# Kernel optimization log

Hardware: AMD Instinct MI355X
Metric: run time of the kernel (lower is better)

The kernel has to match this reference:

```python
import jax, jax.numpy as jnp
import numpy as np
import math

SCALES = (1, 2, 4)
GROUPS = 8
EPS = 1e-5
TEMPERATURE = 1.0


def bilinear_resize(x, out_h, out_w):
    # torch F.interpolate mode='bilinear', align_corners=False
    B, C, h, w = x.shape
    def coords(out, in_):
        c = (jnp.arange(out, dtype=x.dtype) + 0.5) * (in_ / out) - 0.5
        c = jnp.clip(c, 0.0, in_ - 1.0)
        i0 = jnp.floor(c).astype(jnp.int32)
        i1 = jnp.minimum(i0 + 1, in_ - 1)
        t = c - i0.astype(x.dtype)
        return i0, i1, t
    y0, y1, ty = coords(out_h, h)
    x0, x1, tx = coords(out_w, w)
    r0 = x[:, :, y0, :]
    r1 = x[:, :, y1, :]
    v00 = r0[:, :, :, x0]; v01 = r0[:, :, :, x1]
    v10 = r1[:, :, :, x0]; v11 = r1[:, :, :, x1]
    top = v00 * (1.0 - tx) + v01 * tx
    bot = v10 * (1.0 - tx) + v11 * tx
    return top * (1.0 - ty)[:, None] + bot * ty[:, None]


def group_norm(x, gamma, beta):
    B, C, H, W = x.shape
    xg = x.reshape(B, GROUPS, C // GROUPS, H, W)
    mu = xg.mean(axis=(2, 3, 4), keepdims=True)
    var = xg.var(axis=(2, 3, 4), keepdims=True)
    xn = ((xg - mu) * jax.lax.rsqrt(var + EPS)).reshape(B, C, H, W)
    return xn * gamma[None, :, None, None] + beta[None, :, None, None]


def setup_inputs() -> dict:
    key = jax.random.key(0)
    B, C, H, W = 4, 128, 64, 64
    inter = max(C // 4, 8)  # 32
    S = len(SCALES)
    ks = jax.random.split(key, 8)
    def xavier(k, shape, fan_in, fan_out):
        a = math.sqrt(6.0 / (fan_in + fan_out))
        return jax.random.uniform(k, shape, jnp.float32, -a, a)
    inp = {
        'x': jax.random.normal(ks[0], (B, C, H, W), jnp.float32),
        'gn_w': jnp.ones((S, C), jnp.float32),
        'gn_b': jnp.zeros((S, C), jnp.float32),
        'qw': xavier(ks[1], (S, inter, C), C, inter),
        'qb': jnp.zeros((S, inter), jnp.float32),
        'kw': xavier(ks[2], (S, inter, C), C, inter),
        'kb': jnp.zeros((S, inter), jnp.float32),
        'vw': xavier(ks[3], (S, inter, C), C, inter),
        'vb': jnp.zeros((S, inter), jnp.float32),
        'ow': xavier(ks[4], (S, C, inter), inter, C),
        'ob': jnp.zeros((S, C), jnp.float32),
        'gamma': jnp.full((S,), 0.1 / S, jnp.float32),
        'scale_weights': jnp.full((S,), 1.0 / S, jnp.float32),
    }
    return inp


def _forward(x, gn_w, gn_b, qw, qb, kw, kb, vw, vb, ow, ob, gamma, scale_weights):
    B, C, H, W = x.shape
    inter = qw.shape[1]
    inv_scale = 1.0 / (TEMPERATURE * math.sqrt(inter))
    outs = []
    for i, s in enumerate(SCALES):
        if s == 1:
            xs = x
        else:
            xs = x.reshape(B, C, H // s, s, W // s, s).mean(axis=(3, 5))
        h, w = xs.shape[2], xs.shape[3]
        N = h * w
        xn = group_norm(xs, gn_w[i], gn_b[i])
        # 1x1 convs as channel contractions
        q = (jnp.einsum('oc,bchw->bohw', qw[i], xn) + qb[i][None, :, None, None]).reshape(B, inter, N)
        k = (jnp.einsum('oc,bchw->bohw', kw[i], xn) + kb[i][None, :, None, None]).reshape(B, inter, N)
        v = (jnp.einsum('oc,bchw->bohw', vw[i], xn) + vb[i][None, :, None, None]).reshape(B, inter, N)
        logits = jnp.einsum('bin,bim->bnm', q, k) * inv_scale  # [B, N, N]
        attn = jax.nn.softmax(logits, axis=-1)
        att = jnp.einsum('bnm,bim->bin', attn, v).reshape(B, inter, h, w)
        o = jnp.einsum('ci,bihw->bchw', ow[i], att) + ob[i][None, :, None, None]
        y = gamma[i] * o + xs
        if s > 1:
            y = bilinear_resize(y, H, W)
        outs.append(y)
    wts = jax.nn.softmax(scale_weights, axis=0)
    fused = wts[0] * outs[0]
    for i in range(1, len(outs)):
        fused = fused + wts[i] * outs[i]
    return fused


def reference(x, gn_w, gn_b, qw, qb, kw, kb, vw, vb, ow, ob, gamma, scale_weights):
    return _forward(x, gn_w, gn_b, qw, qb, kw, kb, vw, vb, ow, ob, gamma, scale_weights)
```

## Files before the change

### kernel.cpp

```cpp
#include <hip/hip_runtime.h>
#include <math.h>

#define B 4
#define C 128
#define CPG 16
#define INTER 32
#define SPLIT 16
#define KS 4

#define N1 4096
#define N2 1024
#define N4 256

#define QOFF2 (B * N1 * 32)
#define QOFF4 (QOFF2 + B * N2 * 32)
#define QTOT  (QOFF4 + B * N4 * 32)
#define PAOFF2 (B * KS * 32 * N1)
#define PAOFF4 (PAOFF2 + B * KS * 32 * N2)
#define PATOT  (PAOFF4 + B * KS * 32 * N4)
#define PMOFF2 (B * KS * 2 * N1)
#define PMOFF4 (PMOFF2 + B * KS * 2 * N2)
#define PMTOT  (PMOFF4 + B * KS * 2 * N4)

typedef unsigned short ushort_t;
typedef __attribute__((ext_vector_type(8))) short short8;
typedef __attribute__((ext_vector_type(4))) short short4v;
typedef __attribute__((ext_vector_type(4))) float f32x4;

__device__ __forceinline__ ushort_t f2bf(float f) {
    union { float f; unsigned u; } x; x.f = f;
    unsigned r = x.u + 0x7fffu + ((x.u >> 16) & 1u);
    return (ushort_t)(r >> 16);
}

__device__ __forceinline__ void scale_wts(const float* __restrict__ sw,
                                          float& w0, float& w1, float& w2) {
    float a = sw[0], b = sw[1], c = sw[2];
    float m = fmaxf(a, fmaxf(b, c));
    float e0 = __expf(a - m), e1 = __expf(b - m), e2 = __expf(c - m);
    float inv = 1.0f / (e0 + e1 + e2);
    w0 = e0 * inv; w1 = e1 * inv; w2 = e2 * inv;
}

__device__ __forceinline__ void block_reduce_write(float s, float q,
                                                   float* __restrict__ dst2) {
    __shared__ float rs[256], rq[256];
    rs[threadIdx.x] = s; rq[threadIdx.x] = q;
    __syncthreads();
    for (int st = 128; st > 0; st >>= 1) {
        if (threadIdx.x < st) {
            rs[threadIdx.x] += rs[threadIdx.x + st];
            rq[threadIdx.x] += rq[threadIdx.x + st];
        }
        __syncthreads();
    }
    if (threadIdx.x == 0) { dst2[0] = rs[0]; dst2[1] = rq[0]; }
}

__global__ __launch_bounds__(256) void pool_stats_kernel(const float* __restrict__ x,
                                                         float* __restrict__ xs2,
                                                         float* __restrict__ xs4,
                                                         float* __restrict__ part) {
    int bid = blockIdx.x;
    if (bid < 512) {
        int sp = bid & 15, bg = bid >> 4;
        const float* base = x + ((bg * CPG) << 12) + sp * 4096;
        float s = 0.0f, q = 0.0f;
        for (int i = threadIdx.x; i < 4096; i += 256) {
            float v = base[i];
            s += v; q += v * v;
        }
        block_reduce_write(s, q, part + bid * 2);
    } else if (bid < 1024) {
        int blk = bid - 512;
        int sp = blk & 15, bg = blk >> 4;
        int bc = bg * CPG + sp;
        const float* src = x + (bc << 12);
        float* dst = xs2 + (bc << 10);
        float s = 0.0f, q = 0.0f;
        for (int p = threadIdx.x; p < 1024; p += 256) {
            int oy = p >> 5, ox = p & 31;
            const float* s2 = src + oy * 128 + ox * 2;
            float v = (s2[0] + s2[1] + s2[64] + s2[65]) * 0.25f;
            dst[p] = v; s += v; q += v * v;
        }
        block_reduce_write(s, q, part + 1024 + blk * 2);
    } else {
        int blk = bid - 1024;
        int sp = blk & 15, bg = blk >> 4;
        int bc = bg * CPG + sp;
        const float* src = x + (bc << 12);
        float* dst = xs4 + (bc << 8);
        int p = threadIdx.x & 255;
        int oy = p >> 4, ox = p & 15;
        const float* s4 = src + oy * 256 + ox * 4;
        float v = 0.0f;
        #pragma unroll
        for (int dy = 0; dy < 4; ++dy)
            #pragma unroll
            for (int dx = 0; dx < 4; ++dx) v += s4[dy * 64 + dx];
        v *= 0.0625f;
        dst[p] = v;
        block_reduce_write(v, v * v, part + 2048 + blk * 2);
    }
}

template <int N, int NSH>
__device__ __forceinline__ void qkv_body(int bi, const float* __restrict__ xs,
    const float* __restrict__ part,
    const float* __restrict__ gn_w, const float* __restrict__ gn_b,
    const float* __restrict__ qw, const float* __restrict__ qb,
    const float* __restrict__ kw, const float* __restrict__ kb,
    const float* __restrict__ vw, const float* __restrict__ vb,
    ushort_t* __restrict__ q_bf, ushort_t* __restrict__ k_bf, ushort_t* __restrict__ v_bf) {
    const int nc = N >> 8;
    int nchunk = bi % nc; bi /= nc;
    int og = bi & 3; bi >>= 2;
    int proj = bi % 3; int b = bi / 3;
    const float* wp = (proj == 0) ? qw : ((proj == 1) ? kw : vw);
    const float* bp = (proj == 0) ? qb : ((proj == 1) ? kb : vb);
    __shared__ float wl[8 * 128];
    __shared__ float2 ss[128];
    {
        int t = threadIdx.x;
        #pragma unroll
        for (int r = 0; r < 4; ++r) {
            int e = r * 256 + t;
            int o = e >> 7, c0 = e & 127;
            wl[c0 * 8 + o] = wp[(og * 8 + o) * C + c0];
        }
        if (t < 128) {
            int c = t;
            int bg = b * 8 + (c >> 4);
            float s = 0.0f, q = 0.0f;
            #pragma unroll
            for (int sp = 0; sp < SPLIT; ++sp) {
                s += part[(bg * SPLIT + sp) * 2];
                q += part[(bg * SPLIT + sp) * 2 + 1];
            }
            float inv = 1.0f / (float)(CPG << NSH);
            float mu = s * inv;
            float var = q * inv - mu * mu;
            float a = rsqrtf(var + 1e-5f) * gn_w[c];
            float2 r; r.x = a; r.y = gn_b[c] - mu * a;
            ss[c] = r;
        }
    }
    __syncthreads();
    int n = nchunk * 256 + threadIdx.x;
    const float* xb = xs + ((size_t)(b * C) << NSH) + n;
    float acc[8];
    #pragma unroll
    for (int o = 0; o < 8; ++o) acc[o] = bp[og * 8 + o];
    #pragma unroll 2
    for (int c0 = 0; c0 < C; ++c0) {
        float raw = xb[(size_t)c0 << NSH];
        float2 s2 = ss[c0];
        float xv = fmaf(s2.x, raw, s2.y);
        const float4* wr = (const float4*)&wl[c0 * 8];
        float4 w0 = wr[0], w1 = wr[1];
        acc[0] += w0.x * xv; acc[1] += w0.y * xv; acc[2] += w0.z * xv; acc[3] += w0.w * xv;
        acc[4] += w1.x * xv; acc[5] += w1.y * xv; acc[6] += w1.z * xv; acc[7] += w1.w * xv;
    }
    if (proj < 2) {
        ushort_t tmp[8];
        #pragma unroll
        for (int o = 0; o < 8; ++o) tmp[o] = f2bf(acc[o]);
        ushort_t* dst = ((proj == 0) ? q_bf : k_bf) + ((size_t)(b * N + n)) * 32 + og * 8;
        *(uint4*)dst = *(const uint4*)tmp;
    } else {
        #pragma unroll
        for (int o = 0; o < 8; ++o)
            v_bf[((size_t)(b * 32 + og * 8 + o) << NSH) + n] = f2bf(acc[o]);
    }
}

__global__ __launch_bounds__(256) void qkv_all_kernel(const float* __restrict__ x,
    const float* __restrict__ xs2, const float* __restrict__ xs4,
    const float* __restrict__ part,
    const float* __restrict__ gn_w, const float* __restrict__ gn_b,
    const float* __restrict__ qw, const float* __restrict__ qb,
    const float* __restrict__ kw, const float* __restrict__ kb,
    const float* __restrict__ vw, const float* __restrict__ vb,
    ushort_t* __restrict__ qbf, ushort_t* __restrict__ kbf, ushort_t* __restrict__ vbf) {
    int bid = blockIdx.x;
    if (bid < 768) {
        qkv_body<N1, 12>(bid, x, part, gn_w, gn_b, qw, qb, kw, kb, vw, vb, qbf, kbf, vbf);
    } else if (bid < 960) {
        qkv_body<N2, 10>(bid - 768, xs2, part + 1024, gn_w + C, gn_b + C,
                         qw + INTER * C, qb + INTER, kw + INTER * C, kb + INTER,
                         vw + INTER * C, vb + INTER,
                         qbf + QOFF2, kbf + QOFF2, vbf + QOFF2);
    } else {
        qkv_body<N4, 8>(bid - 960, xs4, part + 2048, gn_w + 2 * C, gn_b + 2 * C,
                        qw + 2 * INTER * C, qb + 2 * INTER, kw + 2 * INTER * C, kb + 2 * INTER,
                        vw + 2 * INTER * C, vb + 2 * INTER,
                        qbf + QOFF4, kbf + QOFF4, vbf + QOFF4);
    }
}

template <int N, int NSH>
__device__ __forceinline__ void attn_body(int bi,
    const ushort_t* __restrict__ q_bf, const ushort_t* __restrict__ k_bf,
    const ushort_t* __restrict__ v_bf,
    float* __restrict__ pacc, float* __restrict__ pml,
    ushort_t* K_lds, ushort_t* V_lds, ushort_t* P_lds) {
    int ks = bi % KS; bi /= KS;
    const int nqc = N >> 6;
    int qc = bi % nqc; int b = bi / nqc;
    int tid = threadIdx.x;
    int l = tid & 63, w = tid >> 6, lq = l & 15, g = l >> 4;
    int q0 = qc * 64 + w * 16;
    const float invs = 0.17677669529663687f * 1.4426950408889634f;

    short8 qf = *(const short8*)(q_bf + ((size_t)(b * N + q0 + lq)) * 32 + g * 8);
    f32x4 acco0 = {0.f, 0.f, 0.f, 0.f}, acco1 = {0.f, 0.f, 0.f, 0.f};
    float mrun = -3.0e38f, lrun = 0.0f;

    const int kchunk = N / KS;
    int kbase = ks * kchunk;
    const int ntiles = kchunk >> 6;
    ushort_t* Pw = P_lds + w * 16 * 72;

    const uint4* ksrc = (const uint4*)(k_bf + ((size_t)(b * N + kbase + (tid >> 2))) * 32 + (tid & 3) * 8);
    const uint4* vsrc = (const uint4*)(v_bf + (((size_t)(b * 32 + (tid >> 3))) << NSH) + kbase + (tid & 7) * 8);
    uint4 kreg = *ksrc, vreg = *vsrc;

    for (int t = 0; t < ntiles; ++t) {
        __syncthreads();
        *(uint4*)&K_lds[(tid >> 2) * 40 + (tid & 3) * 8] = kreg;
        *(uint4*)&V_lds[(tid >> 3) * 72 + (tid & 7) * 8] = vreg;
        __syncthreads();
        if (t + 1 < ntiles) {
            ksrc += 256; vsrc += 8;
            kreg = *ksrc; vreg = *vsrc;
        }

        f32x4 sa[4];
        #pragma unroll
        for (int kt = 0; kt < 4; ++kt) {
            short8 kf = *(const short8*)&K_lds[(kt * 16 + lq) * 40 + g * 8];
            f32x4 z = {0.f, 0.f, 0.f, 0.f};
            sa[kt] = __builtin_amdgcn_mfma_f32_16x16x32_bf16(kf, qf, z, 0, 0, 0);
        }
        float sc[16];
        #pragma unroll
        for (int kt = 0; kt < 4; ++kt) {
            sc[kt * 4 + 0] = sa[kt][0] * invs;
            sc[kt * 4 + 1] = sa[kt][1] * invs;
            sc[kt * 4 + 2] = sa[kt][2] * invs;
            sc[kt * 4 + 3] = sa[kt][3] * invs;
        }
        float tmax = sc[0];
        #pragma unroll
        for (int j = 1; j < 16; ++j) tmax = fmaxf(tmax, sc[j]);
        tmax = fmaxf(tmax, __shfl_xor(tmax, 16, 64));
        tmax = fmaxf(tmax, __shfl_xor(tmax, 32, 64));
        float nm = fmaxf(mrun, tmax);
        float corr = exp2f(mrun - nm);
        float psum = 0.0f;
        ushort_t pb[16];
        #pragma unroll
        for (int j = 0; j < 16; ++j) {
            float p = exp2f(sc[j] - nm);
            psum += p;
            pb[j] = f2bf(p);
        }
        psum += __shfl_xor(psum, 16, 64);
        psum += __shfl_xor(psum, 32, 64);
        lrun = lrun * corr + psum;
        mrun = nm;
        #pragma unroll
        for (int e = 0; e < 4; ++e) { acco0[e] *= corr; acco1[e] *= corr; }
        #pragma unroll
        for (int kt = 0; kt < 4; ++kt) {
            short4v pv4;
            pv4[0] = (short)pb[kt * 4 + 0];
            pv4[1] = (short)pb[kt * 4 + 1];
            pv4[2] = (short)pb[kt * 4 + 2];
            pv4[3] = (short)pb[kt * 4 + 3];
            *(short4v*)&Pw[lq * 72 + kt * 16 + g * 4] = pv4;
        }
        #pragma unroll
        for (int c = 0; c < 2; ++c) {
            short8 pf  = *(const short8*)&Pw[lq * 72 + c * 32 + g * 8];
            short8 vf0 = *(const short8*)&V_lds[(lq) * 72 + c * 32 + g * 8];
            short8 vf1 = *(const short8*)&V_lds[(16 + lq) * 72 + c * 32 + g * 8];
            acco0 = __builtin_amdgcn_mfma_f32_16x16x32_bf16(vf0, pf, acco0, 0, 0, 0);
            acco1 = __builtin_amdgcn_mfma_f32_16x16x32_bf16(vf1, pf, acco1, 0, 0, 0);
        }
    }
    int n = q0 + lq;
    size_t pb_ = ((size_t)(b * KS + ks)) * 32;
    #pragma unroll
    for (int r = 0; r < 4; ++r) {
        pacc[(pb_ + (g * 4 + r)) * N + n]      = acco0[r];
        pacc[(pb_ + 16 + (g * 4 + r)) * N + n] = acco1[r];
    }
    if (g == 0) {
        pml[((size_t)(b * KS + ks) * 2) * N + n]     = mrun;
        pml[((size_t)(b * KS + ks) * 2 + 1) * N + n] = lrun;
    }
}

__global__ __launch_bounds__(256) void attn_all_kernel(
    const ushort_t* __restrict__ qbf, const ushort_t* __restrict__ kbf,
    const ushort_t* __restrict__ vbf,
    float* __restrict__ pacc, float* __restrict__ pml) {
    __shared__ ushort_t K_lds[64 * 40];
    __shared__ ushort_t V_lds[32 * 72];
    __shared__ ushort_t P_lds[4 * 16 * 72];
    int bid = blockIdx.x;
    if (bid < 1024) {
        attn_body<N1, 12>(bid, qbf, kbf, vbf, pacc, pml, K_lds, V_lds, P_lds);
    } else if (bid < 1280) {
        attn_body<N2, 10>(bid - 1024, qbf + QOFF2, kbf + QOFF2, vbf + QOFF2,
                          pacc + PAOFF2, pml + PMOFF2, K_lds, V_lds, P_lds);
    } else {
        attn_body<N4, 8>(bid - 1280, qbf + QOFF4, kbf + QOFF4, vbf + QOFF4,
                         pacc + PAOFF4, pml + PMOFF4, K_lds, V_lds, P_lds);
    }
}

template <int N, int NSH>
__device__ __forceinline__ void comb_oy_body(int tile, const float* __restrict__ pacc,
    const float* __restrict__ pml, const float* __restrict__ ow, const float* __restrict__ ob,
    const float* __restrict__ gamma, const float* __restrict__ xs,
    float* __restrict__ ydst, const float* __restrict__ sw,
    float* att_lds, float* ow_lds) {
    const int ntiles = N >> 5;
    int b = tile / ntiles;
    int n0 = (tile % ntiles) << 5;
    int t = threadIdx.x;
    {
        const float4* src = (const float4*)ow;
        float4* dst = (float4*)ow_lds;
        dst[t] = src[t]; dst[256 + t] = src[256 + t];
        dst[512 + t] = src[512 + t]; dst[768 + t] = src[768 + t];
    }
    {
        int o = t >> 3, j = t & 7;
        int n = n0 + j * 4;
        float4 mv[KS], lv[KS], av4[KS];
        float4 M = {-3.0e38f, -3.0e38f, -3.0e38f, -3.0e38f};
        #pragma unroll
        for (int k2 = 0; k2 < KS; ++k2) {
            mv[k2]  = *(const float4*)&pml[((size_t)(b * KS + k2) * 2) * N + n];
            lv[k2]  = *(const float4*)&pml[((size_t)(b * KS + k2) * 2 + 1) * N + n];
            av4[k2] = *(const float4*)&pacc[((size_t)(b * KS + k2) * INTER + o) * N + n];
            M.x = fmaxf(M.x, mv[k2].x); M.y = fmaxf(M.y, mv[k2].y);
            M.z = fmaxf(M.z, mv[k2].z); M.w = fmaxf(M.w, mv[k2].w);
        }
        float4 L = {0.f, 0.f, 0.f, 0.f}, A = {0.f, 0.f, 0.f, 0.f};
        #pragma unroll
        for (int k2 = 0; k2 < KS; ++k2) {
            float4 wg;
            wg.x = exp2f(mv[k2].x - M.x); wg.y = exp2f(mv[k2].y - M.y);
            wg.z = exp2f(mv[k2].z - M.z); wg.w = exp2f(mv[k2].w - M.w);
            L.x += lv[k2].x * wg.x; L.y += lv[k2].y * wg.y;
            L.z += lv[k2].z * wg.z; L.w += lv[k2].w * wg.w;
            A.x += av4[k2].x * wg.x; A.y += av4[k2].y * wg.y;
            A.z += av4[k2].z * wg.z; A.w += av4[k2].w * wg.w;
        }
        float4 r;
        r.x = A.x / L.x; r.y = A.y / L.y; r.z = A.z / L.z; r.w = A.w / L.w;
        *(float4*)&att_lds[o * 36 + j * 4] = r;
    }
    __syncthreads();
    {
        int n = t & 31, cg2 = t >> 5;
        float av[32];
        #pragma unroll
        for (int i = 0; i < 32; ++i) av[i] = att_lds[i * 36 + n];
        float gm = gamma[0];
        float wsc = 1.0f;
        if (sw) { float w0, w1, w2; scale_wts(sw, w0, w1, w2); wsc = w0; }
        const float* xsb = xs + ((size_t)(b * C + cg2 * 16) << NSH) + n0 + n;
        float* yb = ydst + ((size_t)(b * C + cg2 * 16) << NSH) + n0 + n;
        #pragma unroll 4
        for (int cc = 0; cc < 16; ++cc) {
            int c = cg2 * 16 + cc;
            const float4* wr = (const float4*)&ow_lds[c * 32];
            float a0 = 0.f, a1 = 0.f, a2 = 0.f, a3 = 0.f;
            #pragma unroll
            for (int i4 = 0; i4 < 8; ++i4) {
                float4 wv = wr[i4];
                a0 += wv.x * av[i4 * 4 + 0]; a1 += wv.y * av[i4 * 4 + 1];
                a2 += wv.z * av[i4 * 4 + 2]; a3 += wv.w * av[i4 * 4 + 3];
            }
            float o_ = ob[c] + ((a0 + a1) + (a2 + a3));
            float y = gm * o_ + xsb[(size_t)cc << NSH];
            yb[(size_t)cc << NSH] = wsc * y;
        }
    }
    __syncthreads();
}

__global__ __launch_bounds__(256) void comb_oy_all_kernel(const float* __restrict__ pacc,
    const float* __restrict__ pml,
    const float* __restrict__ ow, const float* __restrict__ ob,
    const float* __restrict__ gamma,
    const float* __restrict__ x, const float* __restrict__ xs2, const float* __restrict__ xs4,
    float* __restrict__ out, float* __restrict__ y2, float* __restrict__ y4,
    const float* __restrict__ sw) {
    __shared__ float att_lds[32 * 36];
    __shared__ float ow_lds[128 * 32];
    int bid = blockIdx.x;
    if (bid < 512) {
        comb_oy_body<N1, 12>(bid, pacc, pml, ow, ob, gamma, x, out, sw, att_lds, ow_lds);
    } else if (bid < 640) {
        comb_oy_body<N2, 10>(bid - 512, pacc + PAOFF2, pml + PMOFF2,
                             ow + C * INTER, ob + C, gamma + 1, xs2, y2, nullptr,
                             att_lds, ow_lds);
    } else {
        comb_oy_body<N4, 8>(bid - 640, pacc + PAOFF4, pml + PMOFF4,
                            ow + 2 * C * INTER, ob + 2 * C, gamma + 2, xs4, y4, nullptr,
                            att_lds, ow_lds);
    }
}

__device__ __forceinline__ float bilerp(const float* __restrict__ img, int in,
                                        int oy, int ox, float r) {
    float cy = (oy + 0.5f) * r - 0.5f;
    cy = fminf(fmaxf(cy, 0.0f), (float)(in - 1));
    float cx = (ox + 0.5f) * r - 0.5f;
    cx = fminf(fmaxf(cx, 0.0f), (float)(in - 1));
    int y0 = (int)cy; int y1i = (y0 + 1 < in) ? y0 + 1 : in - 1; float ty = cy - (float)y0;
    int x0 = (int)cx; int x1i = (x0 + 1 < in) ? x0 + 1 : in - 1; float tx = cx - (float)x0;
    float v00 = img[y0 * in + x0];
    float v01 = img[y0 * in + x1i];
    float v10 = img[y1i * in + x0];
    float v11 = img[y1i * in + x1i];
    float top = v00 * (1.0f - tx) + v01 * tx;
    float bot = v10 * (1.0f - tx) + v11 * tx;
    return top * (1.0f - ty) + bot * ty;
}

__global__ __launch_bounds__(256) void fuse_kernel(float* __restrict__ out,
                                                   const float* __restrict__ y2,
                                                   const float* __restrict__ y4,
                                                   const float* __restrict__ sw) {
    int idx = blockIdx.x * 256 + threadIdx.x;
    int p = idx & 4095;
    int bc = idx >> 12;
    int oy = p >> 6, ox = p & 63;
    float w0, w1, w2; scale_wts(sw, w0, w1, w2);
    float v2 = bilerp(y2 + bc * 1024, 32, oy, ox, 0.5f);
    float v4 = bilerp(y4 + bc * 256, 16, oy, ox, 0.25f);
    out[idx] = out[idx] + w1 * v2 + w2 * v4;
}

extern "C" void kernel_launch(void* const* d_in, const int* in_sizes, int n_in,
                              void* d_out, int out_size, void* d_ws, size_t ws_size,
                              hipStream_t stream) {
    const float* x     = (const float*)d_in[0];
    const float* gn_w  = (const float*)d_in[1];
    const float* gn_b  = (const float*)d_in[2];
    const float* qw    = (const float*)d_in[3];
    const float* qb    = (const float*)d_in[4];
    const float* kw    = (const float*)d_in[5];
    const float* kb    = (const float*)d_in[6];
    const float* vw    = (const float*)d_in[7];
    const float* vb    = (const float*)d_in[8];
    const float* ow    = (const float*)d_in[9];
    const float* ob    = (const float*)d_in[10];
    const float* gamma = (const float*)d_in[11];
    const float* sw    = (const float*)d_in[12];
    float* out = (float*)d_out;

    float* ws    = (float*)d_ws;
    float* xs2   = ws;
    float* xs4   = xs2 + 524288;
    float* y2    = xs4 + 131072;
    float* y4    = y2 + 524288;
    float* part  = y4 + 131072;
    float* pacc  = part + 3072;
    float* pml   = pacc + PATOT;
    ushort_t* qbf = (ushort_t*)(pml + PMTOT);
    ushort_t* kbf = qbf + QTOT;
    ushort_t* vbf = kbf + QTOT;

    pool_stats_kernel<<<1536, 256, 0, stream>>>(x, xs2, xs4, part);
    qkv_all_kernel<<<1008, 256, 0, stream>>>(x, xs2, xs4, part, gn_w, gn_b,
                                             qw, qb, kw, kb, vw, vb, qbf, kbf, vbf);
    attn_all_kernel<<<1344, 256, 0, stream>>>(qbf, kbf, vbf, pacc, pml);
    comb_oy_all_kernel<<<672, 256, 0, stream>>>(pacc, pml, ow, ob, gamma,
                                                x, xs2, xs4, out, y2, y4, sw);
    fuse_kernel<<<8192, 256, 0, stream>>>(out, y2, y4, sw);
}
```

Before: 89.30 us.

## Swizzle attention LDS tiles, fold softmax scale into Q, pack bf16 conversion

Replaces the padded LDS layouts for K, V and P with unpadded XOR-swizzled layouts, aiming to avoid bank conflicts while using less shared memory. The softmax scale (1/sqrt(d)·log2e) is now applied to Q before its bf16 conversion in the QKV kernel, which removes a per-score multiply in the attention inner loop. The P probabilities are converted with the hardware packed v_cvt_pk_bf16_f32 instruction instead of software rounding. Rounding the scaled Q to bf16 changes numerics slightly, and the swizzle index math has to match exactly between the writes and the MFMA fragment reads.

```diff
diff --git a/kernel.cpp b/kernel.cpp
--- a/kernel.cpp
+++ b/kernel.cpp
@@ -22,9 +22,10 @@
 #define PMOFF4 (PMOFF2 + B * KS * 2 * N2)
 #define PMTOT  (PMOFF4 + B * KS * 2 * N4)
 
+#define QSCALE 0.25503490f
+
 typedef unsigned short ushort_t;
 typedef __attribute__((ext_vector_type(8))) short short8;
-typedef __attribute__((ext_vector_type(4))) short short4v;
 typedef __attribute__((ext_vector_type(4))) float f32x4;
 
 __device__ __forceinline__ ushort_t f2bf(float f) {
@@ -163,9 +164,10 @@
         acc[4] += w1.x * xv; acc[5] += w1.y * xv; acc[6] += w1.z * xv; acc[7] += w1.w * xv;
     }
     if (proj < 2) {
+        float fs = (proj == 0) ? QSCALE : 1.0f;
         ushort_t tmp[8];
         #pragma unroll
-        for (int o = 0; o < 8; ++o) tmp[o] = f2bf(acc[o]);
+        for (int o = 0; o < 8; ++o) tmp[o] = f2bf(acc[o] * fs);
         ushort_t* dst = ((proj == 0) ? q_bf : k_bf) + ((size_t)(b * N + n)) * 32 + og * 8;
         *(uint4*)dst = *(const uint4*)tmp;
     } else {
@@ -211,7 +213,6 @@
     int tid = threadIdx.x;
     int l = tid & 63, w = tid >> 6, lq = l & 15, g = l >> 4;
     int q0 = qc * 64 + w * 16;
-    const float invs = 0.17677669529663687f * 1.4426950408889634f;
 
     short8 qf = *(const short8*)(q_bf + ((size_t)(b * N + q0 + lq)) * 32 + g * 8);
     f32x4 acco0 = {0.f, 0.f, 0.f, 0.f}, acco1 = {0.f, 0.f, 0.f, 0.f};
@@ -220,16 +221,25 @@
     const int kchunk = N / KS;
     int kbase = ks * kchunk;
     const int ntiles = kchunk >> 6;
-    ushort_t* Pw = P_lds + w * 16 * 72;
-
-    const uint4* ksrc = (const uint4*)(k_bf + ((size_t)(b * N + kbase + (tid >> 2))) * 32 + (tid & 3) * 8);
-    const uint4* vsrc = (const uint4*)(v_bf + (((size_t)(b * 32 + (tid >> 3))) << NSH) + kbase + (tid & 7) * 8);
+    ushort_t* Pw = P_lds + w * 16 * 64;
+
+    const int krow = tid >> 2;
+    const int kidx = krow * 32 + ((((tid & 3) * 16) ^ ((krow & 3) << 4)) >> 1);
+    const int vrow = tid >> 3;
+    const int vidx = vrow * 64 + ((((tid & 7) * 16) ^ ((vrow & 7) << 4)) >> 1);
+
+    const uint4* ksrc = (const uint4*)(k_bf + ((size_t)(b * N + kbase + krow)) * 32 + (tid & 3) * 8);
+    const uint4* vsrc = (const uint4*)(v_bf + (((size_t)(b * 32 + vrow)) << NSH) + kbase + (tid & 7) * 8);
     uint4 kreg = *ksrc, vreg = *vsrc;
+
+    const int ksw = (g ^ (lq & 3)) << 3;
+    const int vsw0 = ((g * 16) ^ ((lq & 7) << 4)) >> 1;
+    const int vsw1 = ((64 + g * 16) ^ ((lq & 7) << 4)) >> 1;
 
     for (int t = 0; t < ntiles; ++t) {
         __syncthreads();
-        *(uint4*)&K_lds[(tid >> 2) * 40 + (tid & 3) * 8] = kreg;
-        *(uint4*)&V_lds[(tid >> 3) * 72 + (tid & 7) * 8] = vreg;
+        *(uint4*)&K_lds[kidx] = kreg;
+        *(uint4*)&V_lds[vidx] = vreg;
         __syncthreads();
         if (t + 1 < ntiles) {
             ksrc += 256; vsrc += 8;
@@ -239,32 +249,32 @@
         f32x4 sa[4];
         #pragma unroll
         for (int kt = 0; kt < 4; ++kt) {
-            short8 kf = *(const short8*)&K_lds[(kt * 16 + lq) * 40 + g * 8];
+            short8 kf = *(const short8*)&K_lds[(kt * 16 + lq) * 32 + ksw];
             f32x4 z = {0.f, 0.f, 0.f, 0.f};
             sa[kt] = __builtin_amdgcn_mfma_f32_16x16x32_bf16(kf, qf, z, 0, 0, 0);
         }
-        float sc[16];
+        float s[16];
         #pragma unroll
         for (int kt = 0; kt < 4; ++kt) {
-            sc[kt * 4 + 0] = sa[kt][0] * invs;
-            sc[kt * 4 + 1] = sa[kt][1] * invs;
-            sc[kt * 4 + 2] = sa[kt][2] * invs;
-            sc[kt * 4 + 3] = sa[kt][3] * invs;
-        }
-        float tmax = sc[0];
-        #pragma unroll
-        for (int j = 1; j < 16; ++j) tmax = fmaxf(tmax, sc[j]);
+            s[kt * 4 + 0] = sa[kt][0]; s[kt * 4 + 1] = sa[kt][1];
+            s[kt * 4 + 2] = sa[kt][2]; s[kt * 4 + 3] = sa[kt][3];
+        }
+        float t0 = fmaxf(fmaxf(s[0], s[1]), s[2]);
+        float t1 = fmaxf(fmaxf(s[3], s[4]), s[5]);
+        float t2 = fmaxf(fmaxf(s[6], s[7]), s[8]);
+        float t3 = fmaxf(fmaxf(s[9], s[10]), s[11]);
+        float t4 = fmaxf(fmaxf(s[12], s[13]), s[14]);
+        float tmax = fmaxf(fmaxf(fmaxf(t0, t1), fmaxf(t2, t3)), fmaxf(t4, s[15]));
         tmax = fmaxf(tmax, __shfl_xor(tmax, 16, 64));
         tmax = fmaxf(tmax, __shfl_xor(tmax, 32, 64));
         float nm = fmaxf(mrun, tmax);
         float corr = exp2f(mrun - nm);
+        float p[16];
         float psum = 0.0f;
-        ushort_t pb[16];
         #pragma unroll
         for (int j = 0; j < 16; ++j) {
-            float p = exp2f(sc[j] - nm);
-            psum += p;
-            pb[j] = f2bf(p);
+            p[j] = exp2f(s[j] - nm);
+            psum += p[j];
         }
         psum += __shfl_xor(psum, 16, 64);
         psum += __shfl_xor(psum, 32, 64);
@@ -274,20 +284,24 @@
         for (int e = 0; e < 4; ++e) { acco0[e] *= corr; acco1[e] *= corr; }
         #pragma unroll
         for (int kt = 0; kt < 4; ++kt) {
-            short4v pv4;
-            pv4[0] = (short)pb[kt * 4 + 0];
-            pv4[1] = (short)pb[kt * 4 + 1];
-            pv4[2] = (short)pb[kt * 4 + 2];
-            pv4[3] = (short)pb[kt * 4 + 3];
-            *(short4v*)&Pw[lq * 72 + kt * 16 + g * 4] = pv4;
-        }
-        #pragma unroll
-        for (int c = 0; c < 2; ++c) {
-            short8 pf  = *(const short8*)&Pw[lq * 72 + c * 32 + g * 8];
-            short8 vf0 = *(const short8*)&V_lds[(lq) * 72 + c * 32 + g * 8];
-            short8 vf1 = *(const short8*)&V_lds[(16 + lq) * 72 + c * 32 + g * 8];
-            acco0 = __builtin_amdgcn_mfma_f32_16x16x32_bf16(vf0, pf, acco0, 0, 0, 0);
-            acco1 = __builtin_amdgcn_mfma_f32_16x16x32_bf16(vf1, pf, acco1, 0, 0, 0);
+            unsigned u01, u23;
+            asm("v_cvt_pk_bf16_f32 %0, %1, %2" : "=v"(u01) : "v"(p[kt * 4 + 0]), "v"(p[kt * 4 + 1]));
+            asm("v_cvt_pk_bf16_f32 %0, %1, %2" : "=v"(u23) : "v"(p[kt * 4 + 2]), "v"(p[kt * 4 + 3]));
+            int poff = kt * 32 + g * 8;
+            uint2 pv; pv.x = u01; pv.y = u23;
+            *(uint2*)&Pw[lq * 64 + ((poff ^ ((lq & 7) << 4)) >> 1)] = pv;
+        }
+        {
+            short8 pf0 = *(const short8*)&Pw[lq * 64 + vsw0];
+            short8 vf00 = *(const short8*)&V_lds[lq * 64 + vsw0];
+            short8 vf10 = *(const short8*)&V_lds[(16 + lq) * 64 + vsw0];
+            acco0 = __builtin_amdgcn_mfma_f32_16x16x32_bf16(vf00, pf0, acco0, 0, 0, 0);
+            acco1 = __builtin_amdgcn_mfma_f32_16x16x32_bf16(vf10, pf0, acco1, 0, 0, 0);
+            short8 pf1 = *(const short8*)&Pw[lq * 64 + vsw1];
+            short8 vf01 = *(const short8*)&V_lds[lq * 64 + vsw1];
+            short8 vf11 = *(const short8*)&V_lds[(16 + lq) * 64 + vsw1];
+            acco0 = __builtin_amdgcn_mfma_f32_16x16x32_bf16(vf01, pf1, acco0, 0, 0, 0);
+            acco1 = __builtin_amdgcn_mfma_f32_16x16x32_bf16(vf11, pf1, acco1, 0, 0, 0);
         }
     }
     int n = q0 + lq;
@@ -307,9 +321,9 @@
     const ushort_t* __restrict__ qbf, const ushort_t* __restrict__ kbf,
     const ushort_t* __restrict__ vbf,
     float* __restrict__ pacc, float* __restrict__ pml) {
-    __shared__ ushort_t K_lds[64 * 40];
-    __shared__ ushort_t V_lds[32 * 72];
-    __shared__ ushort_t P_lds[4 * 16 * 72];
+    __shared__ ushort_t K_lds[64 * 32];
+    __shared__ ushort_t V_lds[32 * 64];
+    __shared__ ushort_t P_lds[4 * 16 * 64];
     int bid = blockIdx.x;
     if (bid < 1024) {
         attn_body<N1, 12>(bid, qbf, kbf, vbf, pacc, pml, K_lds, V_lds, P_lds);
```

Measured after the change: 85.68 us. 1.04x faster.
